# Performance work log

Hardware: AMD Instinct MI355X
Metric: run time of the kernel (lower is better)

The kernel has to match this reference:

```python
import jax, jax.numpy as jnp
import numpy as np

N = 10000      # nodes
E = 320000     # edges
IN = 256       # in_dim == out_dim
H = 8          # heads
D = 32         # head_dim = in_dim // heads
CLAMP = 5.0
BN_EPS = 1e-5


def setup_inputs() -> dict:
    key = jax.random.key(0)
    ks = jax.random.split(key, 24)
    s = 0.05
    nrm = lambda k, shape, sc=s: (jax.random.normal(k, shape, jnp.float32) * sc)
    inp = {
        "x": nrm(ks[0], (N, IN), 1.0),
        "edge_attr": nrm(ks[1], (E, IN), 1.0),
        "log_deg": jax.random.uniform(ks[2], (N, 1), jnp.float32, 0.1, 3.0),
        "edge_index": jax.random.randint(ks[3], (2, E), 0, N, jnp.int32),
        # attention projections (stored [in, out]; x @ W + b)
        "Qw": nrm(ks[4], (IN, H * D)), "Qb": jnp.zeros((H * D,), jnp.float32),
        "Kw": nrm(ks[5], (IN, H * D)), "Kb": jnp.zeros((H * D,), jnp.float32),
        "Ew": nrm(ks[6], (IN, H * D * 2)), "Eb": jnp.zeros((H * D * 2,), jnp.float32),
        "Vw": nrm(ks[7], (IN, H * D)), "Vb": jnp.zeros((H * D,), jnp.float32),
        "Aw": nrm(ks[8], (D, H, 1)),
        "VeRow": nrm(ks[9], (D, H, D)),
        # layer params
        "deg_coef": nrm(ks[10], (1, H * D, 2)),
        "Now": nrm(ks[11], (H * D, IN)), "Nob": jnp.zeros((IN,), jnp.float32),
        "Eow": nrm(ks[12], (H * D, IN)), "Eob": jnp.zeros((IN,), jnp.float32),
        "bn1n_g": jnp.ones((IN,), jnp.float32), "bn1n_b": jnp.zeros((IN,), jnp.float32),
        "bn1e_g": jnp.ones((IN,), jnp.float32), "bn1e_b": jnp.zeros((IN,), jnp.float32),
        "f1w": nrm(ks[13], (IN, 2 * IN)), "f1b": jnp.zeros((2 * IN,), jnp.float32),
        "f2w": nrm(ks[14], (2 * IN, IN)), "f2b": jnp.zeros((IN,), jnp.float32),
        "bn2_g": jnp.ones((IN,), jnp.float32), "bn2_b": jnp.zeros((IN,), jnp.float32),
    }
    return inp


def _bn(x, g, b):
    # batch_norm with batch statistics (bn_no_runner=True => track_running_stats=False)
    mu = jnp.mean(x, axis=0)
    var = jnp.mean(jnp.square(x - mu), axis=0)  # biased, as torch BN
    return (x - mu) * jax.lax.rsqrt(var + BN_EPS) * g + b


def _attention(x, edge_attr, edge_index, Qw, Qb, Kw, Kb, Ew, Eb, Vw, Vb, Aw, VeRow):
    n = x.shape[0]
    src, dst = edge_index[0], edge_index[1]
    Qh = (x @ Qw + Qb).reshape(n, H, D)
    Kh = (x @ Kw + Kb).reshape(n, H, D)
    Vh = (x @ Vw + Vb).reshape(n, H, D)
    Ex = (edge_attr @ Ew + Eb).reshape(-1, H, 2 * D)
    score1 = Kh[src] + Qh[dst]                      # [E,H,D]
    s2 = Ex[:, :, :D] * Ex[:, :, D:]
    score2 = jnp.sign(s2) * jnp.sqrt(jnp.abs(s2))   # == sqrt(relu(s2)) - sqrt(relu(-s2))
    conn = jax.nn.relu(score1 + score2)             # [E,H,D] (attn act='relu')
    score = jnp.einsum('ehd,dhc->ehc', conn, Aw)    # [E,H,1]
    score = jnp.clip(score, -CLAMP, CLAMP)
    # segment softmax over destination nodes
    m = jax.ops.segment_max(score, dst, num_segments=n)
    e = jnp.exp(score - m[dst])
    ssum = jax.ops.segment_sum(e, dst, num_segments=n)
    attn = e / (ssum[dst] + 1e-16)                  # [E,H,1]
    msg = Vh[src] * attn
    Vo = Qh + jax.ops.segment_sum(msg, dst, num_segments=n)
    rowV = jax.ops.segment_sum(conn * attn, dst, num_segments=n)
    rowV = jnp.einsum('nhd,dhc->nhc', rowV, VeRow)
    Vo = Vo + rowV
    return Vo.reshape(n, H * D), conn.reshape(-1, H * D)


def reference(x, edge_attr, log_deg, edge_index, Qw, Qb, Kw, Kb, Ew, Eb, Vw, Vb,
              Aw, VeRow, deg_coef, Now, Nob, Eow, Eob, bn1n_g, bn1n_b,
              bn1e_g, bn1e_b, f1w, f1b, f2w, f2b, bn2_g, bn2_b):
    nh, eh = _attention(x, edge_attr, edge_index, Qw, Qb, Kw, Kb, Ew, Eb, Vw, Vb, Aw, VeRow)
    # degree scaler
    nh = nh * deg_coef[:, :, 0] + (nh * log_deg) * deg_coef[:, :, 1]
    nh = nh @ Now + Nob
    eh = eh @ Eow + Eob
    nh = x + nh
    eh = edge_attr + eh
    nh = _bn(nh, bn1n_g, bn1n_b)
    eh = _bn(eh, bn1e_g, bn1e_b)
    ffn = jax.nn.relu(nh @ f1w + f1b) @ f2w + f2b
    nh = _bn(nh + ffn, bn2_g, bn2_b)
    return nh, eh
```

## Files before the change

kernel.cpp:

```cpp
#include <hip/hip_runtime.h>

#define NN 10000
#define NE 320000

typedef float f4 __attribute__((ext_vector_type(4)));
typedef float f32x4 __attribute__((ext_vector_type(4)));
typedef short bf16x8 __attribute__((ext_vector_type(8)));

__device__ __forceinline__ unsigned short f2b(float f) {
  unsigned u = __float_as_uint(f);
  u += 0x7fff + ((u >> 16) & 1);
  return (unsigned short)(u >> 16);
}
__device__ __forceinline__ float b2f(unsigned short s) {
  return __uint_as_float(((unsigned)s) << 16);
}
__device__ __forceinline__ bf16x8 pack8(f4 a, f4 b) {
  bf16x8 r;
  r[0] = (short)f2b(a[0]); r[1] = (short)f2b(a[1]);
  r[2] = (short)f2b(a[2]); r[3] = (short)f2b(a[3]);
  r[4] = (short)f2b(b[0]); r[5] = (short)f2b(b[1]);
  r[6] = (short)f2b(b[2]); r[7] = (short)f2b(b[3]);
  return r;
}
__device__ __forceinline__ int swz(int row, int k) {
  return (row * 256 + k) ^ ((row & 7) << 3);
}

__global__ void castw_k(const float* __restrict__ in, unsigned short* __restrict__ out,
                        int K, int lg)
{
  int idx = blockIdx.x * 256 + threadIdx.x;
  if (idx >= (K << lg)) return;
  int n = idx & ((1 << lg) - 1), k = idx >> lg;
  out[(size_t)n * K + k] = f2b(in[idx]);
}

__global__ __launch_bounds__(256) void gemm_bf16_k(
    const float* __restrict__ A, const unsigned short* __restrict__ BT,
    const float* __restrict__ bias, const float* __restrict__ res,
    float* __restrict__ C, float* __restrict__ stats,
    int M, int K, int NT, int flags)
{
  __shared__ unsigned short Al[64][40];
  __shared__ unsigned short Bl[128][40];
  const int t = threadIdx.x;
  const int n0 = blockIdx.x * 128;
  const int m0 = blockIdx.y * 64;
  const int lane = t & 63, c = lane & 15, g = lane >> 4, w = t >> 6;
  f32x4 acc[8] = {};
  for (int k0 = 0; k0 < K; k0 += 32) {
    {
      int row = t >> 2, kk = (t & 3) * 8;
      f4 v0 = {0.f,0.f,0.f,0.f}, v1 = {0.f,0.f,0.f,0.f};
      if (m0 + row < M) {
        const f4* p = (const f4*)(A + (size_t)(m0 + row) * K + k0 + kk);
        v0 = p[0]; v1 = p[1];
      }
      __syncthreads();
      *(bf16x8*)&Al[row][kk] = pack8(v0, v1);
    }
    {
      int col = t >> 1, kk = (t & 1) * 16;
      const bf16x8* p = (const bf16x8*)(BT + (size_t)(n0 + col) * K + k0 + kk);
      *(bf16x8*)&Bl[col][kk] = p[0];
      *(bf16x8*)&Bl[col][kk + 8] = p[1];
    }
    __syncthreads();
    bf16x8 a = *(bf16x8*)&Al[w * 16 + c][g * 8];
#pragma unroll
    for (int nb = 0; nb < 8; nb++) {
      bf16x8 b = *(bf16x8*)&Bl[nb * 16 + c][g * 8];
      acc[nb] = __builtin_amdgcn_mfma_f32_16x16x32_bf16(a, b, acc[nb], 0, 0, 0);
    }
  }
  const int do_relu = flags & 1, do_stats = flags & 2;
#pragma unroll
  for (int nb = 0; nb < 8; nb++) {
    const int col = n0 + nb * 16 + c;
    const float bs = bias[col];
    float sn = 0.f, qn = 0.f;
#pragma unroll
    for (int r = 0; r < 4; r++) {
      int row = m0 + w * 16 + g * 4 + r;
      if (row < M) {
        float v = acc[nb][r] + bs;
        if (res) v += res[(size_t)row * NT + col];
        if (do_relu) v = fmaxf(v, 0.f);
        C[(size_t)row * NT + col] = v;
        sn += v; qn += v * v;
      }
    }
    if (do_stats) {
      sn += __shfl_xor(sn, 16); sn += __shfl_xor(sn, 32);
      qn += __shfl_xor(qn, 16); qn += __shfl_xor(qn, 32);
      if (g == 0) {
        atomicAdd(&stats[col], sn);
        atomicAdd(&stats[NT + col], qn);
      }
    }
  }
}

__global__ __launch_bounds__(256) void edge_conn_k(
    const float* __restrict__ EA, const unsigned short* __restrict__ EwT,
    const float* __restrict__ Eb, const float* __restrict__ Kh,
    const float* __restrict__ Qh, const int* __restrict__ ei,
    const float* __restrict__ Aw, float* __restrict__ conn, float* __restrict__ score)
{
  __shared__ unsigned short Abuf[16384];
  __shared__ unsigned short Bbuf[16384];
  float* Exl = (float*)Bbuf;
  const int t = threadIdx.x;
  const int e0 = blockIdx.x * 64;
  const int lane = t & 63, c = lane & 15, g = lane >> 4, w = t >> 6;
#pragma unroll
  for (int it = 0; it < 8; it++) {
    int o = t + it * 256;
    int row = o >> 5, kk = (o & 31) * 8;
    const f4* p = (const f4*)(EA + (size_t)(e0 + row) * 256 + kk);
    f4 v0 = p[0], v1 = p[1];
    *(bf16x8*)&Abuf[swz(row, kk)] = pack8(v0, v1);
  }
  const int m2 = t >> 2, dg = t & 3;
  const int e = e0 + m2;
  const int src = ei[e], dst = ei[NE + e];
  for (int h = 0; h < 8; h++) {
    __syncthreads();
#pragma unroll
    for (int it = 0; it < 8; it++) {
      int o = t + it * 256;
      int row = o >> 5, kk = (o & 31) * 8;
      *(bf16x8*)&Bbuf[swz(row, kk)] =
          *(const bf16x8*)(EwT + (size_t)(h * 64 + row) * 256 + kk);
    }
    __syncthreads();
    f32x4 acc[4] = {};
#pragma unroll
    for (int ks = 0; ks < 8; ks++) {
      bf16x8 a = *(bf16x8*)&Abuf[swz(w * 16 + c, ks * 32 + g * 8)];
#pragma unroll
      for (int cb = 0; cb < 4; cb++) {
        bf16x8 b = *(bf16x8*)&Bbuf[swz(cb * 16 + c, ks * 32 + g * 8)];
        acc[cb] = __builtin_amdgcn_mfma_f32_16x16x32_bf16(a, b, acc[cb], 0, 0, 0);
      }
    }
    __syncthreads();
#pragma unroll
    for (int cb = 0; cb < 4; cb++) {
      float eb = Eb[h * 64 + cb * 16 + c];
#pragma unroll
      for (int r = 0; r < 4; r++)
        Exl[(w * 16 + g * 4 + r) * 68 + cb * 16 + c] = acc[cb][r] + eb;
    }
    __syncthreads();
    const int cb2 = h * 32 + dg * 8;
    const float* ex = Exl + m2 * 68;
    f4 x1a = *(const f4*)(ex + dg * 8);
    f4 x1b = *(const f4*)(ex + dg * 8 + 4);
    f4 x2a = *(const f4*)(ex + 32 + dg * 8);
    f4 x2b = *(const f4*)(ex + 32 + dg * 8 + 4);
    f4 k1 = *(const f4*)(Kh + (size_t)src * 256 + cb2);
    f4 k2 = *(const f4*)(Kh + (size_t)src * 256 + cb2 + 4);
    f4 q1 = *(const f4*)(Qh + (size_t)dst * 256 + cb2);
    f4 q2 = *(const f4*)(Qh + (size_t)dst * 256 + cb2 + 4);
    f4 c1, c2;
    float part = 0.f;
#pragma unroll
    for (int j = 0; j < 4; j++) {
      float s2 = x1a[j] * x2a[j];
      float v = copysignf(sqrtf(fabsf(s2)), s2) + k1[j] + q1[j];
      v = fmaxf(v, 0.f);
      c1[j] = v;
      part += v * Aw[(dg * 8 + j) * 8 + h];
      float s2b = x1b[j] * x2b[j];
      float vb = copysignf(sqrtf(fabsf(s2b)), s2b) + k2[j] + q2[j];
      vb = fmaxf(vb, 0.f);
      c2[j] = vb;
      part += vb * Aw[(dg * 8 + 4 + j) * 8 + h];
    }
    *(f4*)(conn + (size_t)e * 256 + cb2) = c1;
    *(f4*)(conn + (size_t)e * 256 + cb2 + 4) = c2;
    part += __shfl_xor(part, 1);
    part += __shfl_xor(part, 2);
    if (dg == 0) score[(size_t)e * 8 + h] = fminf(fmaxf(part, -5.f), 5.f);
  }
}

__global__ void hist_k(const int* __restrict__ ei, int* __restrict__ cnt)
{
  int e = blockIdx.x * 256 + threadIdx.x;
  if (e < NE) atomicAdd(&cnt[ei[NE + e]], 1);
}

__global__ __launch_bounds__(256) void scan_k(const int* __restrict__ cnt, int* __restrict__ off)
{
  __shared__ int part[256];
  const int t = threadIdx.x;
  const int PER = 40;
  const int base = t * PER;
  int s = 0;
  for (int i = 0; i < PER; i++) {
    int b = base + i;
    if (b < NN) s += cnt[b];
  }
  part[t] = s;
  __syncthreads();
  for (int d = 1; d < 256; d <<= 1) {
    int v = (t >= d) ? part[t - d] : 0;
    __syncthreads();
    part[t] += v;
    __syncthreads();
  }
  int run = (t == 0) ? 0 : part[t - 1];
  for (int i = 0; i < PER; i++) {
    int b = base + i;
    if (b < NN) { off[b] = run; run += cnt[b]; }
  }
  if (t == 255) off[NN] = run;
}

__global__ void scat_k(const int* __restrict__ ei, const int* __restrict__ off,
                       int* __restrict__ cur, int* __restrict__ elist)
{
  int e = blockIdx.x * 256 + threadIdx.x;
  if (e < NE) {
    int d = ei[NE + e];
    int p = atomicAdd(&cur[d], 1);
    elist[off[d] + p] = e;
  }
}

__global__ __launch_bounds__(256) void node_agg_k(
    const int* __restrict__ off, const int* __restrict__ elist,
    const int* __restrict__ ei, const float* __restrict__ score,
    const float* __restrict__ Vh, const float* __restrict__ conn,
    const float* __restrict__ Qh, const float* __restrict__ VeRow,
    const float* __restrict__ deg_coef, const float* __restrict__ log_deg,
    float* __restrict__ nh_a)
{
  const int n = blockIdx.x, t = threadIdx.x;
  const int h = t >> 5;
  __shared__ int eL[128];
  __shared__ int srcL[128];
  __shared__ float sS[128 * 8];
  __shared__ float rA[256];
  const int start = off[n];
  const int deg = off[n + 1] - start;
  float m = -1e30f, ssum = 0.f, vo = 0.f, ro = 0.f;
  for (int c0 = 0; c0 < deg; c0 += 128) {
    const int cn = min(128, deg - c0);
    __syncthreads();
    if (t < cn) {
      int e = elist[start + c0 + t];
      eL[t] = e;
      srcL[t] = ei[e];
    }
    __syncthreads();
    for (int i = t; i < cn * 8; i += 256) sS[i] = score[(size_t)eL[i >> 3] * 8 + (i & 7)];
    __syncthreads();
    float mc = -1e30f;
    for (int i = 0; i < cn; i++) mc = fmaxf(mc, sS[i * 8 + h]);
    float nm = fmaxf(m, mc);
    float sc = __expf(m - nm);
    ssum *= sc; vo *= sc; ro *= sc;
    m = nm;
    for (int i = 0; i < cn; i++) {
      float w = __expf(sS[i * 8 + h] - m);
      ssum += w;
      vo = fmaf(w, Vh[(size_t)srcL[i] * 256 + t], vo);
      ro = fmaf(w, conn[(size_t)eL[i] * 256 + t], ro);
    }
  }
  const float inv = 1.f / (ssum + 1e-16f);
  vo *= inv;
  ro *= inv;
  __syncthreads();
  rA[t] = ro;
  __syncthreads();
  float acc = 0.f;
#pragma unroll
  for (int d = 0; d < 32; d++) acc = fmaf(rA[h * 32 + d], VeRow[d * 256 + t], acc);
  float v = Qh[(size_t)n * 256 + t] + vo + acc;
  const float ld = log_deg[n];
  v = v * (deg_coef[2 * t] + ld * deg_coef[2 * t + 1]);
  nh_a[(size_t)n * 256 + t] = v;
}

__global__ __launch_bounds__(256) void eh_gemm_k(
    const unsigned short* __restrict__ EowT, const float* __restrict__ Eob,
    const float* __restrict__ EA, float* __restrict__ eh, float* __restrict__ stb)
{
  __shared__ unsigned short Al[64][264];
  __shared__ unsigned short Bl[256][40];
  __shared__ float lsum[256], lsq[256];
  const int t = threadIdx.x;
  const int e0 = blockIdx.x * 64;
  const int lane = t & 63, c = lane & 15, g = lane >> 4, w = t >> 6;
  lsum[t] = 0.f; lsq[t] = 0.f;
#pragma unroll
  for (int it = 0; it < 8; it++) {
    int o = t + it * 256;
    int row = o >> 5, kk = (o & 31) * 8;
    const f4* p = (const f4*)(eh + (size_t)(e0 + row) * 256 + kk);
    f4 v0 = p[0], v1 = p[1];
    *(bf16x8*)&Al[row][kk] = pack8(v0, v1);
  }
  f32x4 acc[16] = {};
  for (int ks = 0; ks < 8; ks++) {
    __syncthreads();
#pragma unroll
    for (int it = 0; it < 4; it++) {
      int o = t + it * 256;
      int row = o >> 2, kk = (o & 3) * 8;
      *(bf16x8*)&Bl[row][kk] = *(const bf16x8*)(EowT + (size_t)row * 256 + ks * 32 + kk);
    }
    __syncthreads();
    bf16x8 a = *(bf16x8*)&Al[w * 16 + c][ks * 32 + g * 8];
#pragma unroll
    for (int nb = 0; nb < 16; nb++) {
      bf16x8 b = *(bf16x8*)&Bl[nb * 16 + c][g * 8];
      acc[nb] = __builtin_amdgcn_mfma_f32_16x16x32_bf16(a, b, acc[nb], 0, 0, 0);
    }
  }
#pragma unroll
  for (int nb = 0; nb < 16; nb++) {
    const int col = nb * 16 + c;
    const float eob = Eob[col];
    float sn = 0.f, qn = 0.f;
#pragma unroll
    for (int r = 0; r < 4; r++) {
      size_t row = e0 + w * 16 + g * 4 + r;
      float v = acc[nb][r] + eob + EA[row * 256 + col];
      eh[row * 256 + col] = v;
      sn += v; qn += v * v;
    }
    sn += __shfl_xor(sn, 16); sn += __shfl_xor(sn, 32);
    qn += __shfl_xor(qn, 16); qn += __shfl_xor(qn, 32);
    if (g == 0) { atomicAdd(&lsum[col], sn); atomicAdd(&lsq[col], qn); }
  }
  __syncthreads();
  float* dstb = stb + (size_t)(blockIdx.x & 63) * 512;
  atomicAdd(&dstb[t], lsum[t]);
  atomicAdd(&dstb[256 + t], lsq[t]);
}

__global__ void bn_fin_k(float* __restrict__ st, float invR)
{
  int t = threadIdx.x;
  float mean = st[t] * invR;
  float var = st[256 + t] * invR - mean * mean;
  st[t] = mean;
  st[256 + t] = rsqrtf(var + 1e-5f);
}

__global__ void bn_fin_banked_k(const float* __restrict__ banks, float* __restrict__ st,
                                float invR)
{
  int t = threadIdx.x;
  float s = 0.f, q = 0.f;
  for (int b = 0; b < 64; b++) {
    s += banks[(size_t)b * 512 + t];
    q += banks[(size_t)b * 512 + 256 + t];
  }
  float mean = s * invR;
  float var = q * invR - mean * mean;
  st[t] = mean;
  st[256 + t] = rsqrtf(var + 1e-5f);
}

__global__ void bn_apply_k(const float* __restrict__ X, float* __restrict__ Y,
                           const float* __restrict__ st, const float* __restrict__ g,
                           const float* __restrict__ b, long nvec)
{
  long i = (long)blockIdx.x * 256 + threadIdx.x;
  if (i >= nvec) return;
  int base = (int)(i & 63) * 4;
  f4 x = *(const f4*)(X + i * 4);
  f4 mn = *(const f4*)(st + base);
  f4 rs = *(const f4*)(st + 256 + base);
  f4 gg = *(const f4*)(g + base);
  f4 bb = *(const f4*)(b + base);
  f4 y;
#pragma unroll
  for (int j = 0; j < 4; j++) y[j] = (x[j] - mn[j]) * rs[j] * gg[j] + bb[j];
  *(f4*)(Y + i * 4) = y;
}

extern "C" void kernel_launch(void* const* d_in, const int* in_sizes, int n_in,
                              void* d_out, int out_size, void* d_ws, size_t ws_size,
                              hipStream_t stream)
{
  (void)in_sizes; (void)n_in; (void)out_size; (void)ws_size;
  const float* x        = (const float*)d_in[0];
  const float* edge_attr= (const float*)d_in[1];
  const float* log_deg  = (const float*)d_in[2];
  const int*   ei       = (const int*)d_in[3];
  const float* Qw = (const float*)d_in[4];  const float* Qb = (const float*)d_in[5];
  const float* Kw = (const float*)d_in[6];  const float* Kb = (const float*)d_in[7];
  const float* Ew = (const float*)d_in[8];  const float* Eb = (const float*)d_in[9];
  const float* Vw = (const float*)d_in[10]; const float* Vb = (const float*)d_in[11];
  const float* Aw = (const float*)d_in[12]; const float* VeRow = (const float*)d_in[13];
  const float* deg_coef = (const float*)d_in[14];
  const float* Now = (const float*)d_in[15]; const float* Nob = (const float*)d_in[16];
  const float* Eow = (const float*)d_in[17]; const float* Eob = (const float*)d_in[18];
  const float* bn1n_g = (const float*)d_in[19]; const float* bn1n_b = (const float*)d_in[20];
  const float* bn1e_g = (const float*)d_in[21]; const float* bn1e_b = (const float*)d_in[22];
  const float* f1w = (const float*)d_in[23]; const float* f1b = (const float*)d_in[24];
  const float* f2w = (const float*)d_in[25]; const float* f2b = (const float*)d_in[26];
  const float* bn2_g = (const float*)d_in[27]; const float* bn2_b = (const float*)d_in[28];

  float* out_nh = (float*)d_out;
  float* out_eh = out_nh + (size_t)NN * 256;

  float* ws     = (float*)d_ws;
  float* Qh     = ws;
  float* Kh     = Qh + 2560000;
  float* Vh     = Kh + 2560000;
  float* score  = Vh + 2560000;
  float* nh_a   = score + 2560000;
  float* nh2    = nh_a + 2560000;
  float* ffn1   = nh2 + 2560000;
  float* st1    = ffn1 + 5120000;
  float* st2    = st1 + 512;
  float* st3    = st2 + 512;
  float* stb    = st3 + 512;
  unsigned short* QwT = (unsigned short*)(stb + 64 * 512);
  unsigned short* KwT = QwT + 65536;
  unsigned short* VwT = KwT + 65536;
  unsigned short* NowT= VwT + 65536;
  unsigned short* EowT= NowT + 65536;
  unsigned short* EwT = EowT + 65536;
  unsigned short* f1wT= EwT + 131072;
  unsigned short* f2wT= f1wT + 131072;
  int*   cnt    = (int*)(f2wT + 131072);
  int*   off    = cnt + NN;
  int*   cur    = off + NN + 1;
  int*   elist  = cur + NN;

  hipMemsetAsync(cnt, 0, (size_t)NN * 4, stream);
  hipMemsetAsync(cur, 0, (size_t)NN * 4, stream);
  hipMemsetAsync(st1, 0, (size_t)2 * 512 * 4, stream);
  hipMemsetAsync(stb, 0, (size_t)64 * 512 * 4, stream);

  dim3 blk(256);

  castw_k<<<dim3(256), blk, 0, stream>>>(Qw, QwT, 256, 8);
  castw_k<<<dim3(256), blk, 0, stream>>>(Kw, KwT, 256, 8);
  castw_k<<<dim3(256), blk, 0, stream>>>(Vw, VwT, 256, 8);
  castw_k<<<dim3(256), blk, 0, stream>>>(Now, NowT, 256, 8);
  castw_k<<<dim3(256), blk, 0, stream>>>(Eow, EowT, 256, 8);
  castw_k<<<dim3(512), blk, 0, stream>>>(Ew, EwT, 256, 9);
  castw_k<<<dim3(512), blk, 0, stream>>>(f1w, f1wT, 256, 9);
  castw_k<<<dim3(512), blk, 0, stream>>>(f2w, f2wT, 512, 8);

  hist_k<<<dim3(NE / 256), blk, 0, stream>>>(ei, cnt);
  scan_k<<<dim3(1), blk, 0, stream>>>(cnt, off);
  scat_k<<<dim3(NE / 256), blk, 0, stream>>>(ei, off, cur, elist);

  gemm_bf16_k<<<dim3(2, 157), blk, 0, stream>>>(x, QwT, Qb, nullptr, Qh, nullptr,
                                                NN, 256, 256, 0);
  gemm_bf16_k<<<dim3(2, 157), blk, 0, stream>>>(x, KwT, Kb, nullptr, Kh, nullptr,
                                                NN, 256, 256, 0);
  gemm_bf16_k<<<dim3(2, 157), blk, 0, stream>>>(x, VwT, Vb, nullptr, Vh, nullptr,
                                                NN, 256, 256, 0);

  edge_conn_k<<<dim3(NE / 64), blk, 0, stream>>>(edge_attr, EwT, Eb, Kh, Qh, ei, Aw,
                                                 out_eh, score);

  node_agg_k<<<dim3(NN), blk, 0, stream>>>(off, elist, ei, score, Vh, out_eh,
                                           Qh, VeRow, deg_coef, log_deg, nh_a);

  eh_gemm_k<<<dim3(NE / 64), blk, 0, stream>>>(EowT, Eob, edge_attr, out_eh, stb);
  bn_fin_banked_k<<<dim3(1), blk, 0, stream>>>(stb, st3, 1.0f / NE);
  bn_apply_k<<<dim3(NE * 64 / 256), blk, 0, stream>>>(out_eh, out_eh, st3,
                                                      bn1e_g, bn1e_b, (long)NE * 64);

  gemm_bf16_k<<<dim3(2, 157), blk, 0, stream>>>(nh_a, NowT, Nob, x, out_nh, st1,
                                                NN, 256, 256, 2);
  bn_fin_k<<<dim3(1), blk, 0, stream>>>(st1, 1.0f / NN);
  bn_apply_k<<<dim3(NN * 64 / 256), blk, 0, stream>>>(out_nh, nh2, st1,
                                                      bn1n_g, bn1n_b, (long)NN * 64);
  gemm_bf16_k<<<dim3(4, 157), blk, 0, stream>>>(nh2, f1wT, f1b, nullptr, ffn1, nullptr,
                                                NN, 256, 512, 1);
  gemm_bf16_k<<<dim3(2, 157), blk, 0, stream>>>(ffn1, f2wT, f2b, nh2, out_nh, st2,
                                                NN, 512, 256, 2);
  bn_fin_k<<<dim3(1), blk, 0, stream>>>(st2, 1.0f / NN);
  bn_apply_k<<<dim3(NN * 64 / 256), blk, 0, stream>>>(out_nh, out_nh, st2,
                                                      bn2_g, bn2_b, (long)NN * 64);
}
```

Before: 1.045 ms.

## Double-buffer edge GEMM weights, keep A in registers, parallelize softmax max in node aggregation

The edge_conn kernel now holds the edge_attr tile in registers as bf16 fragments instead of shared memory. It streams the Ew weights through a small double-buffered shared tile in 32 K-steps, and computes the conn/score epilogue straight from the MFMA accumulators, which removes the shared staging buffer. The smaller shared footprint and the launch bound of 4 are meant to raise occupancy and overlap the weight loads with the MFMAs, at the cost of one barrier per step and more scattered Kh/Qh loads. In node_agg, the per-chunk max becomes a warp reduction, the exponentials are computed once into shared memory, and the gather loop is unrolled by four to expose more independent memory loads.

```diff
diff --git a/kernel.cpp b/kernel.cpp
--- a/kernel.cpp
+++ b/kernel.cpp
@@ -11,9 +11,6 @@
   unsigned u = __float_as_uint(f);
   u += 0x7fff + ((u >> 16) & 1);
   return (unsigned short)(u >> 16);
-}
-__device__ __forceinline__ float b2f(unsigned short s) {
-  return __uint_as_float(((unsigned)s) << 16);
 }
 __device__ __forceinline__ bf16x8 pack8(f4 a, f4 b) {
   bf16x8 r;
@@ -23,8 +20,8 @@
   r[6] = (short)f2b(b[2]); r[7] = (short)f2b(b[3]);
   return r;
 }
-__device__ __forceinline__ int swz(int row, int k) {
-  return (row * 256 + k) ^ ((row & 7) << 3);
+__device__ __forceinline__ int swzB(int row, int k) {
+  return row * 64 + (k ^ ((row & 7) << 3));
 }
 
 __global__ void castw_k(const float* __restrict__ in, unsigned short* __restrict__ out,
@@ -102,88 +99,108 @@
   }
 }
 
-__global__ __launch_bounds__(256) void edge_conn_k(
+__global__ __launch_bounds__(256, 4) void edge_conn_k(
     const float* __restrict__ EA, const unsigned short* __restrict__ EwT,
     const float* __restrict__ Eb, const float* __restrict__ Kh,
     const float* __restrict__ Qh, const int* __restrict__ ei,
     const float* __restrict__ Aw, float* __restrict__ conn, float* __restrict__ score)
 {
-  __shared__ unsigned short Abuf[16384];
-  __shared__ unsigned short Bbuf[16384];
-  float* Exl = (float*)Bbuf;
+  __shared__ unsigned short Bbuf[2][4096];
   const int t = threadIdx.x;
   const int e0 = blockIdx.x * 64;
   const int lane = t & 63, c = lane & 15, g = lane >> 4, w = t >> 6;
-#pragma unroll
-  for (int it = 0; it < 8; it++) {
-    int o = t + it * 256;
-    int row = o >> 5, kk = (o & 31) * 8;
-    const f4* p = (const f4*)(EA + (size_t)(e0 + row) * 256 + kk);
-    f4 v0 = p[0], v1 = p[1];
-    *(bf16x8*)&Abuf[swz(row, kk)] = pack8(v0, v1);
-  }
-  const int m2 = t >> 2, dg = t & 3;
-  const int e = e0 + m2;
-  const int src = ei[e], dst = ei[NE + e];
-  for (int h = 0; h < 8; h++) {
-    __syncthreads();
-#pragma unroll
-    for (int it = 0; it < 8; it++) {
-      int o = t + it * 256;
-      int row = o >> 5, kk = (o & 31) * 8;
-      *(bf16x8*)&Bbuf[swz(row, kk)] =
-          *(const bf16x8*)(EwT + (size_t)(h * 64 + row) * 256 + kk);
-    }
-    __syncthreads();
-    f32x4 acc[4] = {};
-#pragma unroll
-    for (int ks = 0; ks < 8; ks++) {
-      bf16x8 a = *(bf16x8*)&Abuf[swz(w * 16 + c, ks * 32 + g * 8)];
+
+  bf16x8 areg[8];
+  {
+    const float* ap = EA + (size_t)(e0 + w * 16 + c) * 256 + g * 8;
+#pragma unroll
+    for (int kc = 0; kc < 8; kc++) {
+      f4 v0 = *(const f4*)(ap + kc * 32);
+      f4 v1 = *(const f4*)(ap + kc * 32 + 4);
+      areg[kc] = pack8(v0, v1);
+    }
+  }
+  int esrc[4], edst[4];
+#pragma unroll
+  for (int r = 0; r < 4; r++) {
+    int e = e0 + w * 16 + g * 4 + r;
+    esrc[r] = ei[e];
+    edst[r] = ei[NE + e];
+  }
+  {
+    int row = t >> 2, kk = (t & 3) * 16;
+    const unsigned short* bp = EwT + (size_t)row * 256 + kk;
+    *(bf16x8*)&Bbuf[0][swzB(row, kk)] = *(const bf16x8*)bp;
+    *(bf16x8*)&Bbuf[0][swzB(row, kk + 8)] = *(const bf16x8*)(bp + 8);
+  }
+  __syncthreads();
+  f32x4 acc[4];
+#pragma unroll
+  for (int cb = 0; cb < 4; cb++)
+#pragma unroll
+    for (int z = 0; z < 4; z++) acc[cb][z] = 0.f;
+
+  for (int step = 0; step < 32; step++) {
+    const int cur = step & 1;
+    const int h = step >> 2, kc = step & 3;
+    if (step + 1 < 32) {
+      int h2 = (step + 1) >> 2, kc2 = (step + 1) & 3;
+      int row = t >> 2, kk = (t & 3) * 16;
+      const unsigned short* bp = EwT + (size_t)(h2 * 64 + row) * 256 + kc2 * 64 + kk;
+      *(bf16x8*)&Bbuf[cur ^ 1][swzB(row, kk)] = *(const bf16x8*)bp;
+      *(bf16x8*)&Bbuf[cur ^ 1][swzB(row, kk + 8)] = *(const bf16x8*)(bp + 8);
+    }
+#pragma unroll
+    for (int kk2 = 0; kk2 < 2; kk2++) {
+      bf16x8 a = areg[kc * 2 + kk2];
 #pragma unroll
       for (int cb = 0; cb < 4; cb++) {
-        bf16x8 b = *(bf16x8*)&Bbuf[swz(cb * 16 + c, ks * 32 + g * 8)];
+        bf16x8 b = *(bf16x8*)&Bbuf[cur][swzB(cb * 16 + c, kk2 * 32 + g * 8)];
         acc[cb] = __builtin_amdgcn_mfma_f32_16x16x32_bf16(a, b, acc[cb], 0, 0, 0);
       }
     }
-    __syncthreads();
-#pragma unroll
-    for (int cb = 0; cb < 4; cb++) {
-      float eb = Eb[h * 64 + cb * 16 + c];
-#pragma unroll
-      for (int r = 0; r < 4; r++)
-        Exl[(w * 16 + g * 4 + r) * 68 + cb * 16 + c] = acc[cb][r] + eb;
-    }
-    __syncthreads();
-    const int cb2 = h * 32 + dg * 8;
-    const float* ex = Exl + m2 * 68;
-    f4 x1a = *(const f4*)(ex + dg * 8);
-    f4 x1b = *(const f4*)(ex + dg * 8 + 4);
-    f4 x2a = *(const f4*)(ex + 32 + dg * 8);
-    f4 x2b = *(const f4*)(ex + 32 + dg * 8 + 4);
-    f4 k1 = *(const f4*)(Kh + (size_t)src * 256 + cb2);
-    f4 k2 = *(const f4*)(Kh + (size_t)src * 256 + cb2 + 4);
-    f4 q1 = *(const f4*)(Qh + (size_t)dst * 256 + cb2);
-    f4 q2 = *(const f4*)(Qh + (size_t)dst * 256 + cb2 + 4);
-    f4 c1, c2;
-    float part = 0.f;
-#pragma unroll
-    for (int j = 0; j < 4; j++) {
-      float s2 = x1a[j] * x2a[j];
-      float v = copysignf(sqrtf(fabsf(s2)), s2) + k1[j] + q1[j];
-      v = fmaxf(v, 0.f);
-      c1[j] = v;
-      part += v * Aw[(dg * 8 + j) * 8 + h];
-      float s2b = x1b[j] * x2b[j];
-      float vb = copysignf(sqrtf(fabsf(s2b)), s2b) + k2[j] + q2[j];
-      vb = fmaxf(vb, 0.f);
-      c2[j] = vb;
-      part += vb * Aw[(dg * 8 + 4 + j) * 8 + h];
-    }
-    *(f4*)(conn + (size_t)e * 256 + cb2) = c1;
-    *(f4*)(conn + (size_t)e * 256 + cb2 + 4) = c2;
-    part += __shfl_xor(part, 1);
-    part += __shfl_xor(part, 2);
-    if (dg == 0) score[(size_t)e * 8 + h] = fminf(fmaxf(part, -5.f), 5.f);
+    if (kc == 3) {
+      float eb1[2], eb2[2], aw[2];
+      eb1[0] = Eb[h * 64 + c];      eb1[1] = Eb[h * 64 + 16 + c];
+      eb2[0] = Eb[h * 64 + 32 + c]; eb2[1] = Eb[h * 64 + 48 + c];
+      aw[0] = Aw[c * 8 + h];        aw[1] = Aw[(16 + c) * 8 + h];
+      float kv[2][4], qv[2][4];
+#pragma unroll
+      for (int j = 0; j < 2; j++)
+#pragma unroll
+        for (int r = 0; r < 4; r++) {
+          kv[j][r] = Kh[(size_t)esrc[r] * 256 + h * 32 + j * 16 + c];
+          qv[j][r] = Qh[(size_t)edst[r] * 256 + h * 32 + j * 16 + c];
+        }
+      float p[4] = {0.f, 0.f, 0.f, 0.f};
+#pragma unroll
+      for (int j = 0; j < 2; j++)
+#pragma unroll
+        for (int r = 0; r < 4; r++) {
+          float ex1 = acc[j][r] + eb1[j];
+          float ex2 = acc[j + 2][r] + eb2[j];
+          float s2 = ex1 * ex2;
+          float cv = copysignf(sqrtf(fabsf(s2)), s2) + kv[j][r] + qv[j][r];
+          cv = fmaxf(cv, 0.f);
+          conn[(size_t)(e0 + w * 16 + g * 4 + r) * 256 + h * 32 + j * 16 + c] = cv;
+          p[r] = fmaf(cv, aw[j], p[r]);
+        }
+#pragma unroll
+      for (int r = 0; r < 4; r++) {
+        float v = p[r];
+        v += __shfl_xor(v, 1);
+        v += __shfl_xor(v, 2);
+        v += __shfl_xor(v, 4);
+        v += __shfl_xor(v, 8);
+        if (c == 0)
+          score[(size_t)(e0 + w * 16 + g * 4 + r) * 8 + h] = fminf(fmaxf(v, -5.f), 5.f);
+      }
+#pragma unroll
+      for (int cb = 0; cb < 4; cb++)
+#pragma unroll
+        for (int z = 0; z < 4; z++) acc[cb][z] = 0.f;
+    }
+    __syncthreads();
   }
 }
 
@@ -243,7 +260,8 @@
   const int h = t >> 5;
   __shared__ int eL[128];
   __shared__ int srcL[128];
-  __shared__ float sS[128 * 8];
+  __shared__ float sS[1024];
+  __shared__ float mS[8];
   __shared__ float rA[256];
   const int start = off[n];
   const int deg = off[n + 1] - start;
@@ -260,16 +278,41 @@
     for (int i = t; i < cn * 8; i += 256) sS[i] = score[(size_t)eL[i >> 3] * 8 + (i & 7)];
     __syncthreads();
     float mc = -1e30f;
-    for (int i = 0; i < cn; i++) mc = fmaxf(mc, sS[i * 8 + h]);
+    for (int i = (t & 31); i < cn; i += 32) mc = fmaxf(mc, sS[i * 8 + h]);
+    mc = fmaxf(mc, __shfl_xor(mc, 1));
+    mc = fmaxf(mc, __shfl_xor(mc, 2));
+    mc = fmaxf(mc, __shfl_xor(mc, 4));
+    mc = fmaxf(mc, __shfl_xor(mc, 8));
+    mc = fmaxf(mc, __shfl_xor(mc, 16));
     float nm = fmaxf(m, mc);
+    if ((t & 31) == 0) mS[h] = nm;
+    __syncthreads();
+    for (int i = t; i < cn * 8; i += 256) sS[i] = __expf(sS[i] - mS[i & 7]);
+    __syncthreads();
     float sc = __expf(m - nm);
     ssum *= sc; vo *= sc; ro *= sc;
     m = nm;
-    for (int i = 0; i < cn; i++) {
-      float w = __expf(sS[i * 8 + h] - m);
-      ssum += w;
-      vo = fmaf(w, Vh[(size_t)srcL[i] * 256 + t], vo);
-      ro = fmaf(w, conn[(size_t)eL[i] * 256 + t], ro);
+    int i = 0;
+    for (; i + 4 <= cn; i += 4) {
+      float w0 = sS[(i + 0) * 8 + h], w1 = sS[(i + 1) * 8 + h];
+      float w2 = sS[(i + 2) * 8 + h], w3 = sS[(i + 3) * 8 + h];
+      int s0 = srcL[i], s1 = srcL[i + 1], s2 = srcL[i + 2], s3 = srcL[i + 3];
+      int f0 = eL[i], f1 = eL[i + 1], f2 = eL[i + 2], f3 = eL[i + 3];
+      ssum += w0 + w1 + w2 + w3;
+      vo = fmaf(w0, Vh[(size_t)s0 * 256 + t], vo);
+      vo = fmaf(w1, Vh[(size_t)s1 * 256 + t], vo);
+      vo = fmaf(w2, Vh[(size_t)s2 * 256 + t], vo);
+      vo = fmaf(w3, Vh[(size_t)s3 * 256 + t], vo);
+      ro = fmaf(w0, conn[(size_t)f0 * 256 + t], ro);
+      ro = fmaf(w1, conn[(size_t)f1 * 256 + t], ro);
+      ro = fmaf(w2, conn[(size_t)f2 * 256 + t], ro);
+      ro = fmaf(w3, conn[(size_t)f3 * 256 + t], ro);
+    }
+    for (; i < cn; i++) {
+      float w0 = sS[i * 8 + h];
+      ssum += w0;
+      vo = fmaf(w0, Vh[(size_t)srcL[i] * 256 + t], vo);
+      ro = fmaf(w0, conn[(size_t)eL[i] * 256 + t], ro);
     }
   }
   const float inv = 1.f / (ssum + 1e-16f);
```

Measured after the change: 1.178 ms. 1.13x slower.
